# Performance work log

Hardware: AMD Instinct MI355X
Metric: run time of the kernel (lower is better)

Reference implementation:

```python
import jax, jax.numpy as jnp
import numpy as np
import math

B, T, D, H = 2, 2048, 1024, 16
HD = D // H
EPS = 1e-5


def setup_inputs() -> dict:
    key = jax.random.key(0)
    ks = jax.random.split(key, 8)
    s = 0.02
    return {
        "x": jax.random.normal(ks[0], (B, T, D), dtype=jnp.float32),
        "w_attn": jax.random.normal(ks[1], (D, 3 * D), dtype=jnp.float32) * s,
        "w_proj": jax.random.normal(ks[2], (D, D), dtype=jnp.float32) * s,
        "w_fc": jax.random.normal(ks[3], (D, 4 * D), dtype=jnp.float32) * s,
        "w_out": jax.random.normal(ks[4], (4 * D, D), dtype=jnp.float32) * s,
        "ln1_g": jnp.ones((D,), jnp.float32),
        "ln1_b": jnp.zeros((D,), jnp.float32),
        "ln2_g": jnp.ones((D,), jnp.float32),
        "ln2_b": jnp.zeros((D,), jnp.float32),
    }


def _layernorm(x, g, b):
    mu = jnp.mean(x, axis=-1, keepdims=True)
    var = jnp.var(x, axis=-1, keepdims=True)
    return (x - mu) * jax.lax.rsqrt(var + EPS) * g + b


def _attention(x, w_attn, w_proj):
    qkv = x @ w_attn  # [B, T, 3D]
    q, k, v = jnp.split(qkv, 3, axis=-1)
    # [B, H, T, HD]
    q = q.reshape(B, T, H, HD).transpose(0, 2, 1, 3)
    k = k.reshape(B, T, H, HD).transpose(0, 2, 1, 3)
    v = v.reshape(B, T, H, HD).transpose(0, 2, 1, 3)
    att = jnp.einsum('bhqd,bhkd->bhqk', q, k) * (1.0 / math.sqrt(HD))
    causal = jnp.tril(jnp.ones((T, T), dtype=bool))
    att = jnp.where(causal, att, -jnp.inf)
    att = jax.nn.softmax(att, axis=-1)
    y = jnp.einsum('bhqk,bhkd->bhqd', att, v)
    y = y.transpose(0, 2, 1, 3).reshape(B, T, D)
    return y @ w_proj


def reference(x, w_attn, w_proj, w_fc, w_out, ln1_g, ln1_b, ln2_g, ln2_b):
    x = x + _attention(_layernorm(x, ln1_g, ln1_b), w_attn, w_proj)
    h = _layernorm(x, ln2_g, ln2_b)
    h = jax.nn.gelu(h @ w_fc, approximate=False) @ w_out
    return x + h
```

## Files before the change

### kernel.cpp

```cpp
#include <hip/hip_runtime.h>

typedef short s16x8 __attribute__((ext_vector_type(8)));
typedef float f32x4 __attribute__((ext_vector_type(4)));

#define MFMA16(a, b, c) __builtin_amdgcn_mfma_f32_16x16x32_bf16((a), (b), (c), 0, 0, 0)

__device__ __forceinline__ float b2f(unsigned short u) {
    union { unsigned int i; float f; } c;
    c.i = ((unsigned int)u) << 16;
    return c.f;
}
__device__ __forceinline__ unsigned short f2b(float f) {
    union { float f; unsigned int i; } c;
    c.f = f;
    unsigned int i = c.i + 0x7FFFu + ((c.i >> 16) & 1u);
    return (unsigned short)(i >> 16);
}

__device__ __forceinline__ void gl_lds16(const unsigned short* g, unsigned short* l) {
    __builtin_amdgcn_global_load_lds(
        (const __attribute__((address_space(1))) void*)g,
        (__attribute__((address_space(3))) void*)l, 16, 0, 0);
}

__device__ __forceinline__ float gelu_f(float v) {
    float u2 = 1.5957691216057308f * v * (1.0f + 0.044715f * v * v);
    float t = __expf(fminf(u2, 80.0f));
    return v * t * __builtin_amdgcn_rcpf(t + 1.0f);
}

static constexpr size_t OFF_WAT = 0;
static constexpr size_t OFF_WPT = OFF_WAT + 6291456;
static constexpr size_t OFF_WFT = OFF_WPT + 2097152;
static constexpr size_t OFF_WOT = OFF_WFT + 8388608;
static constexpr size_t OFF_R1  = OFF_WOT + 8388608;
static constexpr size_t OFF_R2  = OFF_R1 + 8388608;
static constexpr size_t OFF_VT  = OFF_R2 + 25165824;
static constexpr size_t OFF_Y   = OFF_VT + 8388608;
static constexpr size_t OFF_X2  = OFF_Y + 8388608;

__global__ __launch_bounds__(256) void prep_kernel(const float* __restrict__ wA,
                                                   const float* __restrict__ wP,
                                                   const float* __restrict__ wF,
                                                   const float* __restrict__ wO,
                                                   unsigned short* __restrict__ WaT,
                                                   unsigned short* __restrict__ WpT,
                                                   unsigned short* __restrict__ WfT,
                                                   unsigned short* __restrict__ WoT,
                                                   const float* __restrict__ x,
                                                   const float* __restrict__ g1,
                                                   const float* __restrict__ b1,
                                                   unsigned short* __restrict__ xn1) {
    __shared__ unsigned short tile[32][33];
    __shared__ float red[2][4];
    const int bb = blockIdx.x;
    if (bb >= 12288) {
        const int row = bb - 12288;
        const int t = threadIdx.x;
        float4 f = ((const float4*)(x + (size_t)row * 1024))[t];
        float v[4] = {f.x, f.y, f.z, f.w};
        float s = v[0] + v[1] + v[2] + v[3];
        float ss = v[0] * v[0] + v[1] * v[1] + v[2] * v[2] + v[3] * v[3];
#pragma unroll
        for (int o = 32; o >= 1; o >>= 1) {
            s += __shfl_down(s, o);
            ss += __shfl_down(ss, o);
        }
        const int wv = t >> 6, ln = t & 63;
        if (ln == 0) { red[0][wv] = s; red[1][wv] = ss; }
        __syncthreads();
        s = red[0][0] + red[0][1] + red[0][2] + red[0][3];
        ss = red[1][0] + red[1][1] + red[1][2] + red[1][3];
        const float mu = s * (1.0f / 1024.0f);
        const float rs = rsqrtf(ss * (1.0f / 1024.0f) - mu * mu + 1e-5f);
        float4 gg = ((const float4*)g1)[t];
        float4 bbv = ((const float4*)b1)[t];
        ushort4 o4;
        o4.x = f2b((v[0] - mu) * rs * gg.x + bbv.x);
        o4.y = f2b((v[1] - mu) * rs * gg.y + bbv.y);
        o4.z = f2b((v[2] - mu) * rs * gg.z + bbv.z);
        o4.w = f2b((v[3] - mu) * rs * gg.w + bbv.w);
        ((ushort4*)(xn1 + (size_t)row * 1024))[t] = o4;
        return;
    }
    const float* W;
    unsigned short* Wt;
    int K, N, rel;
    if (bb < 3072)      { W = wA; Wt = WaT; K = 1024; N = 3072; rel = bb; }
    else if (bb < 4096) { W = wP; Wt = WpT; K = 1024; N = 1024; rel = bb - 3072; }
    else if (bb < 8192) { W = wF; Wt = WfT; K = 1024; N = 4096; rel = bb - 4096; }
    else                { W = wO; Wt = WoT; K = 4096; N = 1024; rel = bb - 8192; }
    const int ntx = N >> 5;
    const int n0 = (rel % ntx) * 32, k0 = (rel / ntx) * 32;
    const int tx = threadIdx.x & 31, ty = threadIdx.x >> 5;
#pragma unroll
    for (int i = 0; i < 32; i += 8)
        tile[ty + i][tx] = f2b(W[(size_t)(k0 + ty + i) * N + (n0 + tx)]);
    __syncthreads();
#pragma unroll
    for (int i = 0; i < 32; i += 8)
        Wt[(size_t)(n0 + ty + i) * K + (k0 + tx)] = tile[tx][ty + i];
}

__global__ __launch_bounds__(256) void ln_kernel(const float* __restrict__ xin,
                                                 const float* __restrict__ gw,
                                                 const float* __restrict__ bw,
                                                 unsigned short* __restrict__ out,
                                                 float* __restrict__ copyf) {
    const int row = blockIdx.x;
    const int t = threadIdx.x;
    float4 f = ((const float4*)(xin + (size_t)row * 1024))[t];
    if (copyf) ((float4*)(copyf + (size_t)row * 1024))[t] = f;
    float v[4] = {f.x, f.y, f.z, f.w};
    float s = v[0] + v[1] + v[2] + v[3];
    float ss = v[0] * v[0] + v[1] * v[1] + v[2] * v[2] + v[3] * v[3];
#pragma unroll
    for (int o = 32; o >= 1; o >>= 1) {
        s += __shfl_down(s, o);
        ss += __shfl_down(ss, o);
    }
    __shared__ float red[2][4];
    const int wv = t >> 6, ln = t & 63;
    if (ln == 0) { red[0][wv] = s; red[1][wv] = ss; }
    __syncthreads();
    s = red[0][0] + red[0][1] + red[0][2] + red[0][3];
    ss = red[1][0] + red[1][1] + red[1][2] + red[1][3];
    const float mu = s * (1.0f / 1024.0f);
    const float rs = rsqrtf(ss * (1.0f / 1024.0f) - mu * mu + 1e-5f);
    float4 gg = ((const float4*)gw)[t];
    float4 bb = ((const float4*)bw)[t];
    ushort4 o4;
    o4.x = f2b((v[0] - mu) * rs * gg.x + bb.x);
    o4.y = f2b((v[1] - mu) * rs * gg.y + bb.y);
    o4.z = f2b((v[2] - mu) * rs * gg.z + bb.z);
    o4.w = f2b((v[3] - mu) * rs * gg.w + bb.w);
    ((ushort4*)(out + (size_t)row * 1024))[t] = o4;
}

template <int EPI, int BN>
__global__ __launch_bounds__(256) void gemm_bt(const unsigned short* __restrict__ A,
                                               const unsigned short* __restrict__ Bt,
                                               void* __restrict__ outp,
                                               const float* __restrict__ residp,
                                               unsigned short* __restrict__ vtp,
                                               int M, int N, int K) {
    constexpr int NWC = (BN == 128) ? 2 : 1;
    constexpr int AI  = (BN == 128) ? 4 : 2;
    constexpr int PB  = BN / 32;
    __shared__ unsigned short As[128 * 64];
    __shared__ unsigned short Bs[BN * 64];
    const int m0 = blockIdx.y * 128, n0 = blockIdx.x * BN;
    const int tid = threadIdx.x;
    const int w = tid >> 6, lane = tid & 63, quad = lane >> 4, lk = lane & 15;
    const int wr = w / NWC, wc = w % NWC;
    const int lrow = lane >> 3, lchunk = lane & 7;
    const int cg = lchunk ^ (lrow & 7);

    const unsigned short* aP = A + (size_t)(m0 + w * 32 + lrow) * K + cg * 8;
    const unsigned short* bP = Bt + (size_t)(n0 + w * (BN / 4) + lrow) * K + cg * 8;
    unsigned short* lA = As + (w * 32) * 64;
    unsigned short* lB = Bs + (w * (BN / 4)) * 64;

    f32x4 acc[AI][4];
#pragma unroll
    for (int i = 0; i < AI; ++i)
#pragma unroll
        for (int j = 0; j < 4; ++j) acc[i][j] = (f32x4){0.f, 0.f, 0.f, 0.f};

    const int kb0 = (EPI == 4) ? blockIdx.z * 16 : 0;
    const int kb1 = (EPI == 4) ? kb0 + 16 : (K >> 6);
    for (int kb = kb0; kb < kb1; ++kb) {
        const unsigned short* aPk = aP + kb * 64;
        const unsigned short* bPk = bP + kb * 64;
#pragma unroll
        for (int p = 0; p < 4; ++p)
            gl_lds16(aPk + (size_t)p * 8 * K, lA + p * 8 * 64);
#pragma unroll
        for (int p = 0; p < PB; ++p)
            gl_lds16(bPk + (size_t)p * 8 * K, lB + p * 8 * 64);
        __syncthreads();
#pragma unroll
        for (int ks = 0; ks < 2; ++ks) {
            const int s = (ks * 4 + quad) ^ (lk & 7);
            s16x8 af[AI], bfv[4];
#pragma unroll
            for (int i = 0; i < AI; ++i)
                af[i] = *(const s16x8*)(As + (wr * (AI * 16) + i * 16 + lk) * 64 + s * 8);
#pragma unroll
            for (int j = 0; j < 4; ++j)
                bfv[j] = *(const s16x8*)(Bs + (wc * 64 + j * 16 + lk) * 64 + s * 8);
#pragma unroll
            for (int i = 0; i < AI; ++i)
#pragma unroll
                for (int j = 0; j < 4; ++j)
                    acc[i][j] = MFMA16(af[i], bfv[j], acc[i][j]);
        }
        __syncthreads();
    }

    const int gr0 = m0 + wr * (AI * 16);
    const int gc0 = n0 + wc * 64;
    if constexpr (EPI == 2) {
#pragma unroll
        for (int i = 0; i < AI; ++i)
#pragma unroll
            for (int r = 0; r < 4; ++r) {
                const int gr = gr0 + i * 16 + quad * 4 + r;
                const size_t ro = (size_t)gr * N;
#pragma unroll
                for (int j = 0; j < 4; ++j) {
                    const int gc = gc0 + j * 16 + lk;
                    ((float*)outp)[ro + gc] = residp[ro + gc] + acc[i][j][r];
                }
            }
    } else if constexpr (EPI == 4) {
#pragma unroll
        for (int i = 0; i < AI; ++i)
#pragma unroll
            for (int r = 0; r < 4; ++r) {
                const int gr = gr0 + i * 16 + quad * 4 + r;
                const size_t ro = (size_t)gr * N;
#pragma unroll
                for (int j = 0; j < 4; ++j) {
                    const int gc = gc0 + j * 16 + lk;
                    unsafeAtomicAdd(&((float*)outp)[ro + gc], acc[i][j][r]);
                }
            }
    } else if (EPI == 3 && gc0 >= 2048) {
        const int h = (gc0 - 2048) >> 6;
        const int bq = m0 >> 11;
        const size_t vb = (size_t)(bq * 16 + h) * 64;
        const int tg0 = (m0 & 2047) + wr * (AI * 16);
        unsigned short* Ept = As + w * 2048;
#pragma unroll
        for (int i = 0; i < AI; ++i) {
#pragma unroll
            for (int j = 0; j < 4; ++j)
#pragma unroll
                for (int r = 0; r < 4; ++r)
                    Ept[(j * 16 + lk) * 24 + quad * 4 + r] = f2b(acc[i][j][r]);
            const int d = lane;
#pragma unroll
            for (int half = 0; half < 2; ++half) {
                uint4 dd = *(const uint4*)(Ept + d * 24 + half * 8);
                *(uint4*)(vtp + (vb + d) * 2048 + tg0 + i * 16 + half * 8) = dd;
            }
        }
    } else {
        unsigned short* Ep = As + w * (16 * 72);
#pragma unroll
        for (int i = 0; i < AI; ++i) {
#pragma unroll
            for (int j = 0; j < 4; ++j)
#pragma unroll
                for (int r = 0; r < 4; ++r) {
                    float v = acc[i][j][r];
                    if constexpr (EPI == 1) v = gelu_f(v);
                    Ep[(quad * 4 + r) * 72 + j * 16 + lk] = f2b(v);
                }
#pragma unroll
            for (int c = 0; c < 2; ++c) {
                const int row = c * 8 + lrow;
                uint4 d = *(const uint4*)(Ep + row * 72 + lchunk * 8);
                const int gr = gr0 + i * 16 + row;
                *(uint4*)((unsigned short*)outp + (size_t)gr * N + gc0 + lchunk * 8) = d;
            }
        }
    }
}

__global__ __launch_bounds__(256) void attn_kernel(const unsigned short* __restrict__ qkv,
                                                   const unsigned short* __restrict__ vt,
                                                   unsigned short* __restrict__ y) {
    __shared__ unsigned short Ks[64 * 64];
    __shared__ unsigned short Vs[64 * 64];
    __shared__ __align__(16) unsigned short Ps[4][2][576];
    const int tid = threadIdx.x;
    const int w = tid >> 6, lane = tid & 63, quad = lane >> 4, lk = lane & 15;
    const int bb = blockIdx.x;
    const int bh = bb & 31;
    const int p = bb >> 5;
    const int b = bh >> 4, h = bh & 15;
    const size_t rowbase = (size_t)b * 2048;
    const size_t vbase = (size_t)bh * 64;
    const int nt = 32 - p;
    const int rq[2] = {p * 64 + w * 16, (31 - p) * 64 + w * 16};

    const int lrow = lane >> 3, lchunk = lane & 7;

    s16x8 qf[2][2];
#pragma unroll
    for (int si = 0; si < 2; ++si)
#pragma unroll
        for (int ks = 0; ks < 2; ++ks) {
            s16x8 q = *(const s16x8*)(qkv + (rowbase + rq[si] + lk) * 3072 + h * 64 +
                                      ks * 32 + quad * 8);
#pragma unroll
            for (int e = 0; e < 8; ++e) {
                union { unsigned int i; float f; } cc;
                cc.i = ((unsigned int)(unsigned short)q[e]) << 16;
                cc.f *= 0.125f;
                q[e] = (short)(cc.i >> 16);
            }
            qf[si][ks] = q;
        }

    f32x4 oacc[2][4];
    float rsum[2][4];
#pragma unroll
    for (int si = 0; si < 2; ++si) {
#pragma unroll
        for (int dj = 0; dj < 4; ++dj) oacc[si][dj] = (f32x4){0.f, 0.f, 0.f, 0.f};
#pragma unroll
        for (int r = 0; r < 4; ++r) rsum[si][r] = 0.f;
    }

    const int srow = w * 16 + lrow;
    const int cgs = lchunk ^ (srow & 7);
    const unsigned short* kgp = qkv + (rowbase + srow) * 3072 + 1024 + h * 64 + cgs * 8;
    const unsigned short* vgp = vt + (vbase + srow) * 2048 + cgs * 8;
    unsigned short* kl = Ks + w * 1024;
    unsigned short* vl = Vs + w * 1024;

    for (int t = 0; t < nt; ++t) {
#pragma unroll
        for (int i = 0; i < 2; ++i) {
            gl_lds16(kgp + ((size_t)t * 64 + i * 8) * 3072, kl + i * 512);
            gl_lds16(vgp + t * 64 + (size_t)i * 8 * 2048, vl + i * 512);
        }
        __syncthreads();
#pragma unroll
        for (int half = 0; half < 2; ++half) {
            const int k0 = t * 64 + half * 32;
            s16x8 kf[2][2], vf[4];
#pragma unroll
            for (int nj = 0; nj < 2; ++nj)
#pragma unroll
                for (int ks = 0; ks < 2; ++ks) {
                    const int row = half * 32 + nj * 16 + lk;
                    const int s = (ks * 4 + quad) ^ (lk & 7);
                    kf[nj][ks] = *(const s16x8*)(Ks + row * 64 + s * 8);
                }
#pragma unroll
            for (int dj = 0; dj < 4; ++dj) {
                const int s = (half * 4 + quad) ^ (lk & 7);
                vf[dj] = *(const s16x8*)(Vs + (dj * 16 + lk) * 64 + s * 8);
            }
#pragma unroll
            for (int si = 0; si < 2; ++si) {
                const int r0 = rq[si];
                if (k0 > r0 + 15) continue;
                const bool domask = (k0 + 31 > r0);
                f32x4 s[2];
                s[0] = (f32x4){0.f, 0.f, 0.f, 0.f};
                s[1] = (f32x4){0.f, 0.f, 0.f, 0.f};
#pragma unroll
                for (int ks = 0; ks < 2; ++ks) {
                    s[0] = MFMA16(qf[si][ks], kf[0][ks], s[0]);
                    s[1] = MFMA16(qf[si][ks], kf[1][ks], s[1]);
                }
                unsigned short* Pw = Ps[w][si];
#pragma unroll
                for (int nj = 0; nj < 2; ++nj)
#pragma unroll
                    for (int r = 0; r < 4; ++r) {
                        float pv = __expf(s[nj][r]);
                        if (domask) {
                            const int key = k0 + nj * 16 + lk;
                            const int row = r0 + quad * 4 + r;
                            if (key > row) pv = 0.f;
                        }
                        union { float f; unsigned int i; } cc;
                        cc.f = pv;
                        cc.i &= 0xFFFF0000u;
                        rsum[si][r] += cc.f;
                        Pw[(quad * 4 + r) * 36 + nj * 16 + lk] = (unsigned short)(cc.i >> 16);
                    }
                const s16x8 af = *(const s16x8*)(Pw + lk * 36 + quad * 8);
#pragma unroll
                for (int dj = 0; dj < 4; ++dj)
                    oacc[si][dj] = MFMA16(af, vf[dj], oacc[si][dj]);
            }
        }
        __syncthreads();
    }

#pragma unroll
    for (int si = 0; si < 2; ++si) {
#pragma unroll
        for (int o = 1; o < 16; o <<= 1)
#pragma unroll
            for (int r = 0; r < 4; ++r) rsum[si][r] += __shfl_xor(rsum[si][r], o);
        float inv[4];
#pragma unroll
        for (int r = 0; r < 4; ++r) inv[r] = 1.0f / rsum[si][r];
        unsigned short* St = Ps[w][0];
#pragma unroll
        for (int dj = 0; dj < 4; ++dj)
#pragma unroll
            for (int r = 0; r < 4; ++r)
                St[(quad * 4 + r) * 72 + dj * 16 + lk] = f2b(oacc[si][dj][r] * inv[r]);
#pragma unroll
        for (int i = 0; i < 2; ++i) {
            const int row = lane >> 2, chk = (lane & 3) + 4 * i;
            uint4 d = *(const uint4*)(St + row * 72 + chk * 8);
            *(uint4*)(y + (rowbase + rq[si] + row) * 1024 + h * 64 + chk * 8) = d;
        }
    }
}

extern "C" void kernel_launch(void* const* d_in, const int* in_sizes, int n_in,
                              void* d_out, int out_size, void* d_ws, size_t ws_size,
                              hipStream_t stream) {
    const float* x   = (const float*)d_in[0];
    const float* wA  = (const float*)d_in[1];
    const float* wP  = (const float*)d_in[2];
    const float* wF  = (const float*)d_in[3];
    const float* wO  = (const float*)d_in[4];
    const float* g1  = (const float*)d_in[5];
    const float* b1  = (const float*)d_in[6];
    const float* g2  = (const float*)d_in[7];
    const float* b2v = (const float*)d_in[8];

    char* ws = (char*)d_ws;
    unsigned short* WaT  = (unsigned short*)(ws + OFF_WAT);
    unsigned short* WpT  = (unsigned short*)(ws + OFF_WPT);
    unsigned short* WfT  = (unsigned short*)(ws + OFF_WFT);
    unsigned short* WoT  = (unsigned short*)(ws + OFF_WOT);
    unsigned short* xn1  = (unsigned short*)(ws + OFF_R1);
    unsigned short* qkv  = (unsigned short*)(ws + OFF_R2);
    unsigned short* gbuf = (unsigned short*)(ws + OFF_R2);
    unsigned short* vt   = (unsigned short*)(ws + OFF_VT);
    unsigned short* y    = (unsigned short*)(ws + OFF_Y);
    float*          x2   = (float*)(ws + OFF_X2);
    unsigned short* h2   = xn1;
    float*          outf = (float*)d_out;

    prep_kernel<<<16384, 256, 0, stream>>>(wA, wP, wF, wO, WaT, WpT, WfT, WoT,
                                           x, g1, b1, xn1);
    gemm_bt<3, 128><<<dim3(24, 32), 256, 0, stream>>>(xn1, WaT, qkv, nullptr, vt,
                                                      4096, 3072, 1024);
    attn_kernel<<<512, 256, 0, stream>>>(qkv, vt, y);
    gemm_bt<2, 64><<<dim3(16, 32), 256, 0, stream>>>(y, WpT, x2, x, nullptr,
                                                     4096, 1024, 1024);
    ln_kernel<<<4096, 256, 0, stream>>>(x2, g2, b2v, h2, outf);
    gemm_bt<1, 128><<<dim3(32, 32), 256, 0, stream>>>(h2, WfT, gbuf, nullptr, nullptr,
                                                      4096, 4096, 1024);
    gemm_bt<4, 128><<<dim3(8, 32, 4), 256, 0, stream>>>(gbuf, WoT, outf, nullptr, nullptr,
                                                        4096, 1024, 4096);
}
```

Baseline: 368.9 us.

## Swizzle GEMM block order per XCD and drop split-K atomics for output GEMM

```diff
diff --git a/kernel.cpp b/kernel.cpp
--- a/kernel.cpp
+++ b/kernel.cpp
@@ -105,12 +105,10 @@
 __global__ __launch_bounds__(256) void ln_kernel(const float* __restrict__ xin,
                                                  const float* __restrict__ gw,
                                                  const float* __restrict__ bw,
-                                                 unsigned short* __restrict__ out,
-                                                 float* __restrict__ copyf) {
+                                                 unsigned short* __restrict__ out) {
     const int row = blockIdx.x;
     const int t = threadIdx.x;
     float4 f = ((const float4*)(xin + (size_t)row * 1024))[t];
-    if (copyf) ((float4*)(copyf + (size_t)row * 1024))[t] = f;
     float v[4] = {f.x, f.y, f.z, f.w};
     float s = v[0] + v[1] + v[2] + v[3];
     float ss = v[0] * v[0] + v[1] * v[1] + v[2] * v[2] + v[3] * v[3];
@@ -149,7 +147,10 @@
     constexpr int PB  = BN / 32;
     __shared__ unsigned short As[128 * 64];
     __shared__ unsigned short Bs[BN * 64];
-    const int m0 = blockIdx.y * 128, n0 = blockIdx.x * BN;
+    const int lin = blockIdx.x;
+    const int xcd = lin & 7, loc = lin >> 3;
+    const int m0 = (xcd * 4 + (loc & 3)) * 128;
+    const int n0 = (loc >> 2) * BN;
     const int tid = threadIdx.x;
     const int w = tid >> 6, lane = tid & 63, quad = lane >> 4, lk = lane & 15;
     const int wr = w / NWC, wc = w % NWC;
@@ -167,9 +168,8 @@
 #pragma unroll
         for (int j = 0; j < 4; ++j) acc[i][j] = (f32x4){0.f, 0.f, 0.f, 0.f};
 
-    const int kb0 = (EPI == 4) ? blockIdx.z * 16 : 0;
-    const int kb1 = (EPI == 4) ? kb0 + 16 : (K >> 6);
-    for (int kb = kb0; kb < kb1; ++kb) {
+    const int KT = K >> 6;
+    for (int kb = 0; kb < KT; ++kb) {
         const unsigned short* aPk = aP + kb * 64;
         const unsigned short* bPk = bP + kb * 64;
 #pragma unroll
@@ -211,19 +211,6 @@
                 for (int j = 0; j < 4; ++j) {
                     const int gc = gc0 + j * 16 + lk;
                     ((float*)outp)[ro + gc] = residp[ro + gc] + acc[i][j][r];
-                }
-            }
-    } else if constexpr (EPI == 4) {
-#pragma unroll
-        for (int i = 0; i < AI; ++i)
-#pragma unroll
-            for (int r = 0; r < 4; ++r) {
-                const int gr = gr0 + i * 16 + quad * 4 + r;
-                const size_t ro = (size_t)gr * N;
-#pragma unroll
-                for (int j = 0; j < 4; ++j) {
-                    const int gc = gc0 + j * 16 + lk;
-                    unsafeAtomicAdd(&((float*)outp)[ro + gc], acc[i][j][r]);
                 }
             }
     } else if (EPI == 3 && gc0 >= 2048) {
@@ -438,14 +425,14 @@
 
     prep_kernel<<<16384, 256, 0, stream>>>(wA, wP, wF, wO, WaT, WpT, WfT, WoT,
                                            x, g1, b1, xn1);
-    gemm_bt<3, 128><<<dim3(24, 32), 256, 0, stream>>>(xn1, WaT, qkv, nullptr, vt,
-                                                      4096, 3072, 1024);
+    gemm_bt<3, 128><<<768, 256, 0, stream>>>(xn1, WaT, qkv, nullptr, vt,
+                                             4096, 3072, 1024);
     attn_kernel<<<512, 256, 0, stream>>>(qkv, vt, y);
-    gemm_bt<2, 64><<<dim3(16, 32), 256, 0, stream>>>(y, WpT, x2, x, nullptr,
-                                                     4096, 1024, 1024);
-    ln_kernel<<<4096, 256, 0, stream>>>(x2, g2, b2v, h2, outf);
-    gemm_bt<1, 128><<<dim3(32, 32), 256, 0, stream>>>(h2, WfT, gbuf, nullptr, nullptr,
-                                                      4096, 4096, 1024);
-    gemm_bt<4, 128><<<dim3(8, 32, 4), 256, 0, stream>>>(gbuf, WoT, outf, nullptr, nullptr,
-                                                        4096, 1024, 4096);
-}
+    gemm_bt<2, 64><<<512, 256, 0, stream>>>(y, WpT, x2, x, nullptr,
+                                            4096, 1024, 1024);
+    ln_kernel<<<4096, 256, 0, stream>>>(x2, g2, b2v, h2);
+    gemm_bt<1, 128><<<1024, 256, 0, stream>>>(h2, WfT, gbuf, nullptr, nullptr,
+                                              4096, 4096, 1024);
+    gemm_bt<2, 64><<<512, 256, 0, stream>>>(gbuf, WoT, outf, x2, nullptr,
+                                            4096, 1024, 4096);
+}
```

Result: faster. 326.9 us (-11.4%).
